# Optimization experiments

Measured on AMD Instinct MI355X. Metric: run time of the kernel, lower is better.

Reference implementation:

```python
import jax, jax.numpy as jnp
import numpy as np

B, N, E = 2, 50000, 800000
IN_CH, SP_CH, OUT_CH, EDGE_CH = 64, 16, 32, 1


def _xavier(k, shape):
    scale = (2.0 / (shape[0] + shape[1])) ** 0.5
    return jax.random.normal(k, shape, dtype=jnp.float32) * scale


def setup_inputs() -> dict:
    key = jax.random.key(0)
    ks = jax.random.split(key, 20)
    return {
        "X": jax.random.normal(ks[0], (B, N, IN_CH), dtype=jnp.float32),
        "edge_index0": jax.random.randint(ks[1], (2, E), 0, N),
        "edge_index1": jax.random.randint(ks[2], (2, E), 0, N),
        "edge_weight0": jax.random.uniform(ks[3], (E, EDGE_CH), dtype=jnp.float32),
        "edge_weight1": jax.random.uniform(ks[4], (E, EDGE_CH), dtype=jnp.float32),
        "res_n_id0": jnp.arange(N),
        "res_n_id1": jnp.arange(N),
        # conv1 params (in=IN_CH, out=SP_CH)
        "value1": _xavier(ks[5], (IN_CH, SP_CH)),
        "key1": _xavier(ks[6], (SP_CH, SP_CH)),
        "query1": _xavier(ks[7], (SP_CH, SP_CH)),
        "we1": _xavier(ks[8], (EDGE_CH, SP_CH)),
        "att_w1": _xavier(ks[9], (3 * SP_CH, 1)),
        "att_b1": jnp.zeros((1,), jnp.float32),
        "cat_w1": _xavier(ks[10], (2 * SP_CH, SP_CH)),
        "cat_b1": jnp.zeros((SP_CH,), jnp.float32),
        # conv2 params (in=SP_CH, out=OUT_CH)
        "value2": _xavier(ks[11], (SP_CH, OUT_CH)),
        "key2": _xavier(ks[12], (OUT_CH, OUT_CH)),
        "query2": _xavier(ks[13], (OUT_CH, OUT_CH)),
        "we2": _xavier(ks[14], (EDGE_CH, OUT_CH)),
        "att_w2": _xavier(ks[15], (3 * OUT_CH, 1)),
        "att_b2": jnp.zeros((1,), jnp.float32),
        "cat_w2": _xavier(ks[16], (2 * OUT_CH, OUT_CH)),
        "cat_b2": jnp.zeros((OUT_CH,), jnp.float32),
    }


def _egnn_conv(Xs, Xd, ei, ef, value, key_w, query_w, we, att_w, att_b, cat_w, cat_b):
    # Xs: [B,Ns,Cin] source nodes, Xd: [B,Nd,Cin] dest nodes, ei: [2,E], ef: [E,edge_ch]
    xs = Xs @ value                       # [B,Ns,C]
    xd = Xd @ value                       # [B,Nd,C]
    e = ef @ we                           # [E,C]
    xj = xs[:, ei[0]]                     # [B,E,C] source gather
    xi = xd[:, ei[1]]                     # [B,E,C] dest gather
    q = xj @ query_w                      # note: original code names are swapped; kept faithful
    k = xi @ key_w
    att_in = jnp.concatenate([k, q, jnp.broadcast_to(e, q.shape)], axis=-1)  # [B,E,3C]
    att = jax.nn.sigmoid(att_in @ att_w + att_b)      # [B,E,1]
    msg = att * xj * jax.nn.sigmoid(e)                # [B,E,C]
    aggr = jnp.zeros(xd.shape, xd.dtype).at[:, ei[1]].add(msg)  # scatter-add over dest
    upd = jnp.concatenate([xd, aggr], axis=-1) @ cat_w + cat_b  # [B,Nd,C]
    return xd + jax.nn.relu(upd)


def reference(X, edge_index0, edge_index1, edge_weight0, edge_weight1,
              res_n_id0, res_n_id1,
              value1, key1, query1, we1, att_w1, att_b1, cat_w1, cat_b1,
              value2, key2, query2, we2, att_w2, att_b2, cat_w2, cat_b2):
    X1 = _egnn_conv(X, X[:, res_n_id0], edge_index0, edge_weight0,
                    value1, key1, query1, we1, att_w1, att_b1, cat_w1, cat_b1)
    X1 = jax.nn.leaky_relu(X1)  # negative_slope 0.01, matches torch default
    X2 = _egnn_conv(X1, X1[:, res_n_id1], edge_index1, edge_weight1,
                    value2, key2, query2, we2, att_w2, att_b2, cat_w2, cat_b2)
    return X2
```

## Files before the change

kernel.cpp:

```cpp
#include <hip/hip_runtime.h>
#include <hip/hip_fp16.h>

#define BB   2
#define NN   50000
#define EE   800000
#define INCH 64
#define C1   16
#define C2   32
#define NB   (BB*NN)

#define W1S   6
#define W2S   5
#define NBK1  ((NN + 63) >> 6)
#define NBK2  ((NN + 31) >> 5)
#define NBKT  (NBK1 + NBK2)
#define EB    4096
#define TPB   1024
#define NEBLK ((2*EE + EB - 1) / EB)

#define OFF_XS1   0
#define OFF_XS2   (OFF_XS1 + NB*C1/2)
#define OFF_DOTK1 (OFF_XS2 + NB*C2/2)
#define OFF_DOTQ1 (OFF_DOTK1 + NB)
#define OFF_DOTK2 (OFF_DOTQ1 + NB)
#define OFF_DOTQ2 (OFF_DOTK2 + NB)
#define OFF_AG1   (OFF_DOTQ2 + NB)
#define OFF_AG2   (OFF_AG1 + NN*32)
#define OFF_BTOT  (OFF_AG2 + NN*64)
#define OFF_BBASE (OFF_BTOT + NBKT)
#define OFF_START (OFF_BBASE + NBKT)
#define OFF_DEG   (OFF_START + 2*NN)
#define OFF_SC    (OFF_DEG + 2*NN)
#define OFF_RECS2 (OFF_SC + 2)
#define OFF_REGION (OFF_RECS2 + 2*EE*2)
#define OFF_RECS   OFF_REGION
#define OFF_BCNT   (OFF_REGION + 2*EE*2)
#define OFF_PREC   OFF_REGION

__device__ __forceinline__ float sigmoidf(float x) {
    return __builtin_amdgcn_rcpf(1.0f + __expf(-x));
}

__global__ void k_sc(const float* __restrict__ we1, const float* __restrict__ aw1,
                     const float* __restrict__ we2, const float* __restrict__ aw2,
                     float* __restrict__ sc) {
    if (threadIdx.x == 0) {
        float e = 0.f;
        for (int j = 0; j < C1; ++j) e += we1[j] * aw1[2*C1+j];
        sc[0] = e;
    }
    if (threadIdx.x == 1) {
        float e = 0.f;
        for (int j = 0; j < C2; ++j) e += we2[j] * aw2[2*C2+j];
        sc[1] = e;
    }
}

__global__ __launch_bounds__(TPB) void k_cnt(
        const int* __restrict__ ei0, const int* __restrict__ ei1,
        unsigned* __restrict__ blockCnt) {
    __shared__ unsigned h[NBKT];
    int tid = threadIdx.x;
    for (int i = tid; i < NBKT; i += TPB) h[i] = 0u;
    __syncthreads();
    int base = blockIdx.x * EB;
#pragma unroll
    for (int j = 0; j < EB/TPB; ++j) {
        int t = base + j*TPB + tid;
        if (t < 2*EE) {
            int bkt;
            if (t < EE) { int dst = ei0[EE + t];      bkt = dst >> W1S; }
            else        { int dst = ei1[EE + t - EE]; bkt = NBK1 + (dst >> W2S); }
            atomicAdd(&h[bkt], 1u);
        }
    }
    __syncthreads();
    unsigned* o = blockCnt + (size_t)blockIdx.x * NBKT;
    for (int i = tid; i < NBKT; i += TPB) o[i] = h[i];
}

__global__ __launch_bounds__(512) void k_scanBkt(
        unsigned* __restrict__ blockCnt, unsigned* __restrict__ bktTot) {
    __shared__ unsigned s[512];
    int tid = threadIdx.x;
    int bkt = blockIdx.x;
    unsigned v = (tid < NEBLK) ? blockCnt[(size_t)tid * NBKT + bkt] : 0u;
    s[tid] = v;
    __syncthreads();
    for (int o = 1; o < 512; o <<= 1) {
        unsigned t = (tid >= o) ? s[tid - o] : 0u;
        __syncthreads();
        s[tid] += t;
        __syncthreads();
    }
    if (tid < NEBLK) blockCnt[(size_t)tid * NBKT + bkt] = s[tid] - v;
    if (tid == 511) bktTot[bkt] = s[511];
}

__global__ __launch_bounds__(1024) void k_scanTot(
        const unsigned* __restrict__ bktTot, unsigned* __restrict__ bucketBase) {
    __shared__ unsigned s[1024];
    int tid = threadIdx.x;
    int base = tid * 3;
    unsigned a0 = (base + 0 < NBKT) ? bktTot[base + 0] : 0u;
    unsigned a1 = (base + 1 < NBKT) ? bktTot[base + 1] : 0u;
    unsigned a2 = (base + 2 < NBKT) ? bktTot[base + 2] : 0u;
    unsigned l = a0 + a1 + a2;
    s[tid] = l;
    __syncthreads();
    for (int o = 1; o < 1024; o <<= 1) {
        unsigned t = (tid >= o) ? s[tid - o] : 0u;
        __syncthreads();
        s[tid] += t;
        __syncthreads();
    }
    unsigned ex = s[tid] - l;
    if (base + 0 < NBKT) bucketBase[base + 0] = ex;
    if (base + 1 < NBKT) bucketBase[base + 1] = ex + a0;
    if (base + 2 < NBKT) bucketBase[base + 2] = ex + a0 + a1;
}

__global__ __launch_bounds__(TPB) void k_permute(
        const int* __restrict__ ei0, const int* __restrict__ ei1,
        const float* __restrict__ ew0, const float* __restrict__ ew1,
        const unsigned* __restrict__ blockOff, const unsigned* __restrict__ bucketBase,
        uint2* __restrict__ recs) {
    __shared__ unsigned off[NBKT];
    __shared__ unsigned cur[NBKT];
    int tid = threadIdx.x;
    const unsigned* bo = blockOff + (size_t)blockIdx.x * NBKT;
    for (int i = tid; i < NBKT; i += TPB) { off[i] = bo[i] + bucketBase[i]; cur[i] = 0u; }
    __syncthreads();
    int base = blockIdx.x * EB;
#pragma unroll
    for (int j = 0; j < EB/TPB; ++j) {
        int t = base + j*TPB + tid;
        if (t >= 2*EE) break;
        int bkt, dl, src; float ef;
        if (t < EE) {
            int dst = ei0[EE + t];
            bkt = dst >> W1S; dl = dst & 63;
            src = ei0[t]; ef = ew0[t];
        } else {
            int e = t - EE;
            int dst = ei1[EE + e];
            bkt = NBK1 + (dst >> W2S); dl = dst & 31;
            src = ei1[e]; ef = ew1[e];
        }
        unsigned pos = off[bkt] + atomicAdd(&cur[bkt], 1u);
        recs[pos] = make_uint2((unsigned)src | ((unsigned)dl << 16), __float_as_uint(ef));
    }
}

__global__ __launch_bounds__(256) void k_sortb(
        const uint2* __restrict__ recs, const unsigned* __restrict__ bktTot,
        const unsigned* __restrict__ bucketBase,
        uint2* __restrict__ recs2, unsigned* __restrict__ startA,
        unsigned* __restrict__ degA) {
    __shared__ unsigned h[64], sOff[64], cur[64];
    int tid = threadIdx.x;
    int bkt = blockIdx.x;
    int lay1 = (bkt < NBK1) ? 1 : 0;
    int ndl  = lay1 ? 64 : 32;
    int nodeBase = lay1 ? (bkt << W1S) : ((bkt - NBK1) << W2S);
    int layOff   = lay1 ? 0 : NN;
    if (tid < 64) h[tid] = 0u;
    __syncthreads();
    unsigned cnt = bktTot[bkt], base = bucketBase[bkt];
    for (unsigned i = tid; i < cnt; i += 256)
        atomicAdd(&h[recs[base + i].x >> 16], 1u);
    __syncthreads();
    if (tid == 0) {
        unsigned run = 0;
        for (int d = 0; d < ndl; ++d) { sOff[d] = run; run += h[d]; }
    }
    __syncthreads();
    if (tid < ndl) {
        cur[tid] = sOff[tid];
        int node = nodeBase + tid;
        if (node < NN) {
            startA[layOff + node] = base + sOff[tid];
            degA[layOff + node]   = h[tid];
        }
    }
    __syncthreads();
    for (unsigned i = tid; i < cnt; i += 256) {
        uint2 r = recs[base + i];
        unsigned dl  = r.x >> 16;
        unsigned src = r.x & 0xffffu;
        unsigned pos = atomicAdd(&cur[dl], 1u);
        unsigned dst = (unsigned)nodeBase + dl;
        recs2[base + pos] = make_uint2(src | (dst << 16), r.y);
    }
}

__global__ __launch_bounds__(256) void k_value1(
        const float* __restrict__ X, const float* __restrict__ value1,
        const float* __restrict__ key1, const float* __restrict__ query1,
        const float* __restrict__ aw1,
        __half* __restrict__ xs1h, float* __restrict__ dotk1, float* __restrict__ dotq1) {
    __shared__ float W[INCH*C1];
    __shared__ float KV[C1], QV[C1];
    int tid = threadIdx.x;
    for (int i = tid; i < INCH*C1; i += 256) W[i] = value1[i];
    if (tid < C1) {
        float kv = 0.f, qv = 0.f;
#pragma unroll
        for (int j = 0; j < C1; ++j) {
            kv += key1[tid*C1+j]   * aw1[j];
            qv += query1[tid*C1+j] * aw1[C1+j];
        }
        KV[tid] = kv; QV[tid] = qv;
    }
    __syncthreads();
    int bn = blockIdx.x * 256 + tid;
    if (bn >= NB) return;
    int b = (bn >= NN) ? 1 : 0;
    int node = bn - b*NN;
    const float4* Xr = (const float4*)(X + (size_t)bn * INCH);
    float acc[C1];
#pragma unroll
    for (int j = 0; j < C1; ++j) acc[j] = 0.f;
#pragma unroll
    for (int v = 0; v < 16; ++v) {
        float4 p = Xr[v];
        float x4[4] = {p.x, p.y, p.z, p.w};
#pragma unroll
        for (int h = 0; h < 4; ++h) {
            int i = v*4 + h;
            float xv = x4[h];
#pragma unroll
            for (int j = 0; j < C1; ++j) acc[j] += xv * W[i*C1+j];
        }
    }
    float dk = 0.f, dq = 0.f;
#pragma unroll
    for (int j = 0; j < C1; ++j) { dk += acc[j]*KV[j]; dq += acc[j]*QV[j]; }
    __half* o = xs1h + ((size_t)node * C1) * 2 + b;
#pragma unroll
    for (int j = 0; j < C1; ++j) o[2*j] = __float2half_rn(acc[j]);
    dotk1[node*2 + b] = dk; dotq1[node*2 + b] = dq;
}

__global__ __launch_bounds__(256) void k_prep(
        const uint2* __restrict__ recs2seg, const float* __restrict__ dotk,
        const float* __restrict__ dotq, const float* __restrict__ ab,
        const float* __restrict__ sc, int scIdx, uint2* __restrict__ prec) {
    int e = blockIdx.x * 256 + threadIdx.x;
    uint2 r = recs2seg[e];
    int src = r.x & 0xffff, dst = r.x >> 16;
    float ef = __uint_as_float(r.y);
    float eb = ef * sc[scIdx] + ab[0];
    float2 dk = *(const float2*)(dotk + dst*2);
    float2 dq = *(const float2*)(dotq + src*2);
    float p0 = sigmoidf(dk.x + dq.x + eb);
    float p1 = sigmoidf(dk.y + dq.y + eb);
    unsigned pu = __builtin_bit_cast(unsigned, __floats2half2_rn(p0, p1));
    unsigned eu = (unsigned)__half_as_ushort(__float2half_rn(ef));
    prec[e] = make_uint2((unsigned)src | (pu << 16),
                         (pu >> 16) | (eu << 16));
}

__global__ __launch_bounds__(256) void k_aggr1f(
        const uint2* __restrict__ prec, const float* __restrict__ we,
        const uint2* __restrict__ xsh,
        const unsigned* __restrict__ startA, const unsigned* __restrict__ degA,
        float* __restrict__ aggrf) {
    int t = blockIdx.x * 256 + threadIdx.x;
    int node = t >> 4, sub = t & 15, cp = sub & 7, h = sub >> 3;
    unsigned s = startA[node];
    unsigned n = degA[node];
    float w0 = we[2*cp], w1 = we[2*cp+1];
    float a0 = 0.f, a1 = 0.f, a2 = 0.f, a3 = 0.f;
    unsigned i = (unsigned)h;
    uint2 r_n = make_uint2(0u, 0u); uint2 xr_n = make_uint2(0u, 0u);
    if (i < n) {
        r_n  = prec[s + i];
        xr_n = xsh[(size_t)(r_n.x & 0xffff)*8 + cp];
    }
    for (; i < n; i += 2) {
        uint2 r = r_n; uint2 xr = xr_n;
        if (i + 2 < n) {
            r_n  = prec[s + i + 2];
            xr_n = xsh[(size_t)(r_n.x & 0xffff)*8 + cp];
        }
        float p0 = __half2float(__ushort_as_half((unsigned short)(r.x >> 16)));
        float p1 = __half2float(__ushort_as_half((unsigned short)(r.y & 0xffff)));
        float ef = __half2float(__ushort_as_half((unsigned short)(r.y >> 16)));
        float se0 = sigmoidf(ef * w0);
        float se1 = sigmoidf(ef * w1);
        float2 f0 = __half22float2(__builtin_bit_cast(__half2, xr.x));
        float2 f1 = __half22float2(__builtin_bit_cast(__half2, xr.y));
        a0 += p0 * se0 * f0.x;
        a1 += p1 * se0 * f0.y;
        a2 += p0 * se1 * f1.x;
        a3 += p1 * se1 * f1.y;
    }
    a0 += __shfl_xor(a0, 8); a1 += __shfl_xor(a1, 8);
    a2 += __shfl_xor(a2, 8); a3 += __shfl_xor(a3, 8);
    if (h == 0)
        ((float4*)aggrf)[(size_t)node*8 + cp] = make_float4(a0, a1, a2, a3);
}

__global__ __launch_bounds__(256) void k_update1(
        const float* __restrict__ cat_w, const float* __restrict__ cat_b,
        const float* __restrict__ value2,
        const float* __restrict__ key2, const float* __restrict__ query2,
        const float* __restrict__ aw2,
        const __half* __restrict__ xs1h, const float* __restrict__ aggr1f,
        __half* __restrict__ xs2h, float* __restrict__ dotk2, float* __restrict__ dotq2) {
    __shared__ float CW[2*C1*C1];
    __shared__ float CB[C1];
    __shared__ float V2[C1*C2];
    __shared__ float KV[C2], QV[C2];
    int tid = threadIdx.x;
    for (int i = tid; i < 2*C1*C1; i += 256) CW[i] = cat_w[i];
    for (int i = tid; i < C1*C2;   i += 256) V2[i] = value2[i];
    if (tid < C1) CB[tid] = cat_b[tid];
    if (tid < C2) {
        float kv = 0.f;
#pragma unroll
        for (int j = 0; j < C2; ++j) kv += key2[tid*C2+j] * aw2[j];
        KV[tid] = kv;
    } else if (tid < 2*C2) {
        int c = tid - C2;
        float qv = 0.f;
#pragma unroll
        for (int j = 0; j < C2; ++j) qv += query2[c*C2+j] * aw2[C2+j];
        QV[c] = qv;
    }
    __syncthreads();
    int bn = blockIdx.x * 256 + tid;
    if (bn >= NB) return;
    int b = (bn >= NN) ? 1 : 0;
    int node = bn - b*NN;
    const __half* xr = xs1h + ((size_t)node*C1)*2 + b;
    const float* agp = aggr1f + (size_t)node*32;
    float xd[C1], ag[C1];
#pragma unroll
    for (int i = 0; i < C1; ++i) xd[i] = __half2float(xr[2*i]);
#pragma unroll
    for (int i = 0; i < C1; ++i) ag[i] = agp[(i>>1)*4 + (i&1)*2 + b];
    float x1[C1];
#pragma unroll
    for (int j = 0; j < C1; ++j) {
        float u = CB[j];
#pragma unroll
        for (int i = 0; i < C1; ++i) {
            u += xd[i] * CW[i*C1 + j];
            u += ag[i] * CW[(C1+i)*C1 + j];
        }
        float o = xd[j] + fmaxf(u, 0.f);
        x1[j] = (o > 0.f) ? o : 0.01f * o;
    }
    float o2[C2];
#pragma unroll
    for (int k = 0; k < C2; ++k) o2[k] = 0.f;
#pragma unroll
    for (int j = 0; j < C1; ++j) {
        float xv = x1[j];
#pragma unroll
        for (int k = 0; k < C2; ++k) o2[k] += xv * V2[j*C2 + k];
    }
    float dk = 0.f, dq = 0.f;
#pragma unroll
    for (int k = 0; k < C2; ++k) { dk += o2[k]*KV[k]; dq += o2[k]*QV[k]; }
    __half* o = xs2h + ((size_t)node*C2)*2 + b;
#pragma unroll
    for (int k = 0; k < C2; ++k) o[2*k] = __float2half_rn(o2[k]);
    dotk2[node*2 + b] = dk; dotq2[node*2 + b] = dq;
}

__global__ __launch_bounds__(256) void k_aggr2f(
        const uint2* __restrict__ prec, const float* __restrict__ we,
        const uint2* __restrict__ xsh,
        const unsigned* __restrict__ startA, const unsigned* __restrict__ degA,
        float* __restrict__ aggrf) {
    int t = blockIdx.x * 256 + threadIdx.x;
    int node = t >> 5, sub = t & 31, cp = sub & 15, h = sub >> 4;
    unsigned s = startA[NN + node] - EE;
    unsigned n = degA[NN + node];
    float w0 = we[2*cp], w1 = we[2*cp+1];
    float a0 = 0.f, a1 = 0.f, a2 = 0.f, a3 = 0.f;
    unsigned i = (unsigned)h;
    uint2 r_n = make_uint2(0u, 0u); uint2 xr_n = make_uint2(0u, 0u);
    if (i < n) {
        r_n  = prec[s + i];
        xr_n = xsh[(size_t)(r_n.x & 0xffff)*16 + cp];
    }
    for (; i < n; i += 2) {
        uint2 r = r_n; uint2 xr = xr_n;
        if (i + 2 < n) {
            r_n  = prec[s + i + 2];
            xr_n = xsh[(size_t)(r_n.x & 0xffff)*16 + cp];
        }
        float p0 = __half2float(__ushort_as_half((unsigned short)(r.x >> 16)));
        float p1 = __half2float(__ushort_as_half((unsigned short)(r.y & 0xffff)));
        float ef = __half2float(__ushort_as_half((unsigned short)(r.y >> 16)));
        float se0 = sigmoidf(ef * w0);
        float se1 = sigmoidf(ef * w1);
        float2 f0 = __half22float2(__builtin_bit_cast(__half2, xr.x));
        float2 f1 = __half22float2(__builtin_bit_cast(__half2, xr.y));
        a0 += p0 * se0 * f0.x;
        a1 += p1 * se0 * f0.y;
        a2 += p0 * se1 * f1.x;
        a3 += p1 * se1 * f1.y;
    }
    a0 += __shfl_xor(a0, 16); a1 += __shfl_xor(a1, 16);
    a2 += __shfl_xor(a2, 16); a3 += __shfl_xor(a3, 16);
    if (h == 0)
        ((float4*)aggrf)[(size_t)node*16 + cp] = make_float4(a0, a1, a2, a3);
}

__global__ __launch_bounds__(256) void k_update2(
        const float* __restrict__ cat_w, const float* __restrict__ cat_b,
        const __half* __restrict__ xs2h, const float* __restrict__ aggr2f,
        float* __restrict__ out) {
    __shared__ float CW[2*C2*C2];
    __shared__ float CB[C2];
    int tid = threadIdx.x;
    for (int i = tid; i < 2*C2*C2; i += 256) CW[i] = cat_w[i];
    if (tid < C2) CB[tid] = cat_b[tid];
    __syncthreads();
    int bn = blockIdx.x * 256 + tid;
    if (bn >= NB) return;
    int b = (bn >= NN) ? 1 : 0;
    int node = bn - b*NN;
    const __half* xr = xs2h + ((size_t)node*C2)*2 + b;
    const float* agp = aggr2f + (size_t)node*64;
    float xd[C2], ag[C2];
#pragma unroll
    for (int i = 0; i < C2; ++i) xd[i] = __half2float(xr[2*i]);
#pragma unroll
    for (int i = 0; i < C2; ++i) ag[i] = agp[(i>>1)*4 + (i&1)*2 + b];
    float o[C2];
#pragma unroll
    for (int k = 0; k < C2; ++k) {
        float u = CB[k];
#pragma unroll
        for (int i = 0; i < C2; ++i) {
            u += xd[i] * CW[i*C2 + k];
            u += ag[i] * CW[(C2+i)*C2 + k];
        }
        o[k] = xd[k] + fmaxf(u, 0.f);
    }
    float4* dst = (float4*)(out + (size_t)bn * C2);
#pragma unroll
    for (int v = 0; v < 8; ++v)
        dst[v] = make_float4(o[4*v], o[4*v+1], o[4*v+2], o[4*v+3]);
}

extern "C" void kernel_launch(void* const* d_in, const int* in_sizes, int n_in,
                              void* d_out, int out_size, void* d_ws, size_t ws_size,
                              hipStream_t stream) {
    const float* X      = (const float*)d_in[0];
    const int*   ei0    = (const int*)d_in[1];
    const int*   ei1    = (const int*)d_in[2];
    const float* ew0    = (const float*)d_in[3];
    const float* ew1    = (const float*)d_in[4];
    const float* value1 = (const float*)d_in[7];
    const float* key1   = (const float*)d_in[8];
    const float* query1 = (const float*)d_in[9];
    const float* we1    = (const float*)d_in[10];
    const float* aw1    = (const float*)d_in[11];
    const float* ab1    = (const float*)d_in[12];
    const float* cw1    = (const float*)d_in[13];
    const float* cb1    = (const float*)d_in[14];
    const float* value2 = (const float*)d_in[15];
    const float* key2   = (const float*)d_in[16];
    const float* query2 = (const float*)d_in[17];
    const float* we2    = (const float*)d_in[18];
    const float* aw2    = (const float*)d_in[19];
    const float* ab2    = (const float*)d_in[20];
    const float* cw2    = (const float*)d_in[21];
    const float* cb2    = (const float*)d_in[22];
    float* ws  = (float*)d_ws;
    float* out = (float*)d_out;

    __half* xs1h = (__half*)(ws + OFF_XS1);
    __half* xs2h = (__half*)(ws + OFF_XS2);
    float* aggr1f = ws + OFF_AG1;
    float* aggr2f = ws + OFF_AG2;
    unsigned* blockCnt   = (unsigned*)(ws + OFF_BCNT);
    unsigned* bktTot     = (unsigned*)(ws + OFF_BTOT);
    unsigned* bucketBase = (unsigned*)(ws + OFF_BBASE);
    unsigned* startA     = (unsigned*)(ws + OFF_START);
    unsigned* degA       = (unsigned*)(ws + OFF_DEG);
    uint2*    recs2      = (uint2*)(ws + OFF_RECS2);
    uint2*    recs       = (uint2*)(ws + OFF_RECS);
    uint2*    prec       = (uint2*)(ws + OFF_PREC);

    k_sc<<<1, 64, 0, stream>>>(we1, aw1, we2, aw2, ws + OFF_SC);

    k_value1<<<(NB+255)/256, 256, 0, stream>>>(X, value1, key1, query1, aw1,
                                               xs1h, ws + OFF_DOTK1, ws + OFF_DOTQ1);

    k_cnt<<<NEBLK, TPB, 0, stream>>>(ei0, ei1, blockCnt);
    k_scanBkt<<<NBKT, 512, 0, stream>>>(blockCnt, bktTot);
    k_scanTot<<<1, 1024, 0, stream>>>(bktTot, bucketBase);
    k_permute<<<NEBLK, TPB, 0, stream>>>(ei0, ei1, ew0, ew1,
                                         blockCnt, bucketBase, recs);
    k_sortb<<<NBKT, 256, 0, stream>>>(recs, bktTot, bucketBase,
                                      recs2, startA, degA);

    k_prep<<<EE/256, 256, 0, stream>>>(recs2, ws + OFF_DOTK1, ws + OFF_DOTQ1,
                                       ab1, ws + OFF_SC, 0, prec);
    k_aggr1f<<<(NN*16)/256, 256, 0, stream>>>(prec, we1, (const uint2*)xs1h,
                                              startA, degA, aggr1f);
    k_update1<<<(NB+255)/256, 256, 0, stream>>>(cw1, cb1, value2, key2, query2, aw2,
                                                xs1h, aggr1f,
                                                xs2h, ws + OFF_DOTK2, ws + OFF_DOTQ2);

    k_prep<<<EE/256, 256, 0, stream>>>(recs2 + EE, ws + OFF_DOTK2, ws + OFF_DOTQ2,
                                       ab2, ws + OFF_SC, 1, prec);
    k_aggr2f<<<(NN*32)/256, 256, 0, stream>>>(prec, we2, (const uint2*)xs2h,
                                              startA, degA, aggr2f);
    k_update2<<<(NB+255)/256, 256, 0, stream>>>(cw2, cb2, xs2h, aggr2f, out);
}
```

Before: 325.3 us.

## Fuse value1 projection into edge counting and layer-1 prep into bucket sort

The node projection, the scalar setup and the per-bucket edge histogram now run in one launch. Within each block, 256 threads compute the node projection while the other 768 build the histogram. The layer-1 attention precompute (sigmoid gates packed as half2 plus the edge feature) is folded into the second sort pass, which writes final packed records straight into recs2. This drops two kernel launches and a full read/write pass over the layer-1 edge records. In exchange, the sort kernel does extra gathers of dotk and dotq, and the fused first kernel has divergent roles inside each block.

```diff
diff --git a/kernel.cpp b/kernel.cpp
--- a/kernel.cpp
+++ b/kernel.cpp
@@ -41,37 +41,84 @@
     return __builtin_amdgcn_rcpf(1.0f + __expf(-x));
 }
 
-__global__ void k_sc(const float* __restrict__ we1, const float* __restrict__ aw1,
-                     const float* __restrict__ we2, const float* __restrict__ aw2,
-                     float* __restrict__ sc) {
-    if (threadIdx.x == 0) {
-        float e = 0.f;
-        for (int j = 0; j < C1; ++j) e += we1[j] * aw1[2*C1+j];
-        sc[0] = e;
-    }
-    if (threadIdx.x == 1) {
-        float e = 0.f;
-        for (int j = 0; j < C2; ++j) e += we2[j] * aw2[2*C2+j];
-        sc[1] = e;
-    }
-}
-
-__global__ __launch_bounds__(TPB) void k_cnt(
+__global__ __launch_bounds__(TPB) void k_value1cnt(
+        const float* __restrict__ X, const float* __restrict__ value1,
+        const float* __restrict__ key1, const float* __restrict__ query1,
+        const float* __restrict__ aw1,
         const int* __restrict__ ei0, const int* __restrict__ ei1,
-        unsigned* __restrict__ blockCnt) {
+        const float* __restrict__ we1, const float* __restrict__ we2,
+        const float* __restrict__ aw2,
+        __half* __restrict__ xs1h, float* __restrict__ dotk1,
+        float* __restrict__ dotq1, unsigned* __restrict__ blockCnt,
+        float* __restrict__ sc) {
+    __shared__ float W[INCH*C1];
+    __shared__ float KV[C1], QV[C1];
     __shared__ unsigned h[NBKT];
     int tid = threadIdx.x;
-    for (int i = tid; i < NBKT; i += TPB) h[i] = 0u;
-    __syncthreads();
-    int base = blockIdx.x * EB;
-#pragma unroll
-    for (int j = 0; j < EB/TPB; ++j) {
-        int t = base + j*TPB + tid;
-        if (t < 2*EE) {
-            int bkt;
-            if (t < EE) { int dst = ei0[EE + t];      bkt = dst >> W1S; }
-            else        { int dst = ei1[EE + t - EE]; bkt = NBK1 + (dst >> W2S); }
-            atomicAdd(&h[bkt], 1u);
+    if (tid < 256) {
+        for (int i = tid; i < INCH*C1; i += 256) W[i] = value1[i];
+        if (tid < C1) {
+            float kv = 0.f, qv = 0.f;
+#pragma unroll
+            for (int j = 0; j < C1; ++j) {
+                kv += key1[tid*C1+j]   * aw1[j];
+                qv += query1[tid*C1+j] * aw1[C1+j];
+            }
+            KV[tid] = kv; QV[tid] = qv;
+        }
+    } else {
+        for (int i = tid - 256; i < NBKT; i += 768) h[i] = 0u;
+        if (blockIdx.x == 0 && tid == 256) {
+            float e = 0.f;
+            for (int j = 0; j < C1; ++j) e += we1[j] * aw1[2*C1+j];
+            sc[0] = e;
+        }
+        if (blockIdx.x == 0 && tid == 257) {
+            float e = 0.f;
+            for (int j = 0; j < C2; ++j) e += we2[j] * aw2[2*C2+j];
+            sc[1] = e;
+        }
+    }
+    __syncthreads();
+    if (tid < 256) {
+        int bn = blockIdx.x * 256 + tid;
+        if (bn < NB) {
+            int b = (bn >= NN) ? 1 : 0;
+            int node = bn - b*NN;
+            const float4* Xr = (const float4*)(X + (size_t)bn * INCH);
+            float acc[C1];
+#pragma unroll
+            for (int j = 0; j < C1; ++j) acc[j] = 0.f;
+#pragma unroll
+            for (int v = 0; v < 16; ++v) {
+                float4 p = Xr[v];
+                float x4[4] = {p.x, p.y, p.z, p.w};
+#pragma unroll
+                for (int hh = 0; hh < 4; ++hh) {
+                    int i = v*4 + hh;
+                    float xv = x4[hh];
+#pragma unroll
+                    for (int j = 0; j < C1; ++j) acc[j] += xv * W[i*C1+j];
+                }
+            }
+            float dk = 0.f, dq = 0.f;
+#pragma unroll
+            for (int j = 0; j < C1; ++j) { dk += acc[j]*KV[j]; dq += acc[j]*QV[j]; }
+            __half* o = xs1h + ((size_t)node * C1) * 2 + b;
+#pragma unroll
+            for (int j = 0; j < C1; ++j) o[2*j] = __float2half_rn(acc[j]);
+            dotk1[node*2 + b] = dk; dotq1[node*2 + b] = dq;
+        }
+    } else {
+        int base = blockIdx.x * EB;
+        for (int j = tid - 256; j < EB; j += 768) {
+            int t = base + j;
+            if (t < 2*EE) {
+                int bkt;
+                if (t < EE) { int dst = ei0[EE + t];      bkt = dst >> W1S; }
+                else        { int dst = ei1[EE + t - EE]; bkt = NBK1 + (dst >> W2S); }
+                atomicAdd(&h[bkt], 1u);
+            }
         }
     }
     __syncthreads();
@@ -152,9 +199,11 @@
     }
 }
 
-__global__ __launch_bounds__(256) void k_sortb(
+__global__ __launch_bounds__(256) void k_sortbp(
         const uint2* __restrict__ recs, const unsigned* __restrict__ bktTot,
         const unsigned* __restrict__ bucketBase,
+        const float* __restrict__ dotk1, const float* __restrict__ dotq1,
+        const float* __restrict__ ab1, const float* __restrict__ sc,
         uint2* __restrict__ recs2, unsigned* __restrict__ startA,
         unsigned* __restrict__ degA) {
     __shared__ unsigned h[64], sOff[64], cur[64];
@@ -184,62 +233,28 @@
         }
     }
     __syncthreads();
+    float ec = sc[0], ab0 = ab1[0];
     for (unsigned i = tid; i < cnt; i += 256) {
         uint2 r = recs[base + i];
         unsigned dl  = r.x >> 16;
         unsigned src = r.x & 0xffffu;
         unsigned pos = atomicAdd(&cur[dl], 1u);
         unsigned dst = (unsigned)nodeBase + dl;
-        recs2[base + pos] = make_uint2(src | (dst << 16), r.y);
-    }
-}
-
-__global__ __launch_bounds__(256) void k_value1(
-        const float* __restrict__ X, const float* __restrict__ value1,
-        const float* __restrict__ key1, const float* __restrict__ query1,
-        const float* __restrict__ aw1,
-        __half* __restrict__ xs1h, float* __restrict__ dotk1, float* __restrict__ dotq1) {
-    __shared__ float W[INCH*C1];
-    __shared__ float KV[C1], QV[C1];
-    int tid = threadIdx.x;
-    for (int i = tid; i < INCH*C1; i += 256) W[i] = value1[i];
-    if (tid < C1) {
-        float kv = 0.f, qv = 0.f;
-#pragma unroll
-        for (int j = 0; j < C1; ++j) {
-            kv += key1[tid*C1+j]   * aw1[j];
-            qv += query1[tid*C1+j] * aw1[C1+j];
-        }
-        KV[tid] = kv; QV[tid] = qv;
-    }
-    __syncthreads();
-    int bn = blockIdx.x * 256 + tid;
-    if (bn >= NB) return;
-    int b = (bn >= NN) ? 1 : 0;
-    int node = bn - b*NN;
-    const float4* Xr = (const float4*)(X + (size_t)bn * INCH);
-    float acc[C1];
-#pragma unroll
-    for (int j = 0; j < C1; ++j) acc[j] = 0.f;
-#pragma unroll
-    for (int v = 0; v < 16; ++v) {
-        float4 p = Xr[v];
-        float x4[4] = {p.x, p.y, p.z, p.w};
-#pragma unroll
-        for (int h = 0; h < 4; ++h) {
-            int i = v*4 + h;
-            float xv = x4[h];
-#pragma unroll
-            for (int j = 0; j < C1; ++j) acc[j] += xv * W[i*C1+j];
-        }
-    }
-    float dk = 0.f, dq = 0.f;
-#pragma unroll
-    for (int j = 0; j < C1; ++j) { dk += acc[j]*KV[j]; dq += acc[j]*QV[j]; }
-    __half* o = xs1h + ((size_t)node * C1) * 2 + b;
-#pragma unroll
-    for (int j = 0; j < C1; ++j) o[2*j] = __float2half_rn(acc[j]);
-    dotk1[node*2 + b] = dk; dotq1[node*2 + b] = dq;
+        if (lay1) {
+            float ef = __uint_as_float(r.y);
+            float eb = ef * ec + ab0;
+            float2 dk = *(const float2*)(dotk1 + dst*2);
+            float2 dq = *(const float2*)(dotq1 + src*2);
+            float p0 = sigmoidf(dk.x + dq.x + eb);
+            float p1 = sigmoidf(dk.y + dq.y + eb);
+            unsigned pu = __builtin_bit_cast(unsigned, __floats2half2_rn(p0, p1));
+            unsigned eu = (unsigned)__half_as_ushort(__float2half_rn(ef));
+            recs2[base + pos] = make_uint2(src | (pu << 16),
+                                           (pu >> 16) | (eu << 16));
+        } else {
+            recs2[base + pos] = make_uint2(src | (dst << 16), r.y);
+        }
+    }
 }
 
 __global__ __launch_bounds__(256) void k_prep(
@@ -488,32 +503,31 @@
     unsigned* degA       = (unsigned*)(ws + OFF_DEG);
     uint2*    recs2      = (uint2*)(ws + OFF_RECS2);
     uint2*    recs       = (uint2*)(ws + OFF_RECS);
-    uint2*    prec       = (uint2*)(ws + OFF_PREC);
-
-    k_sc<<<1, 64, 0, stream>>>(we1, aw1, we2, aw2, ws + OFF_SC);
-
-    k_value1<<<(NB+255)/256, 256, 0, stream>>>(X, value1, key1, query1, aw1,
-                                               xs1h, ws + OFF_DOTK1, ws + OFF_DOTQ1);
-
-    k_cnt<<<NEBLK, TPB, 0, stream>>>(ei0, ei1, blockCnt);
+    uint2*    prec2      = (uint2*)(ws + OFF_PREC);
+
+    k_value1cnt<<<NEBLK, TPB, 0, stream>>>(X, value1, key1, query1, aw1,
+                                           ei0, ei1, we1, we2, aw2,
+                                           xs1h, ws + OFF_DOTK1, ws + OFF_DOTQ1,
+                                           blockCnt, ws + OFF_SC);
+
     k_scanBkt<<<NBKT, 512, 0, stream>>>(blockCnt, bktTot);
     k_scanTot<<<1, 1024, 0, stream>>>(bktTot, bucketBase);
     k_permute<<<NEBLK, TPB, 0, stream>>>(ei0, ei1, ew0, ew1,
                                          blockCnt, bucketBase, recs);
-    k_sortb<<<NBKT, 256, 0, stream>>>(recs, bktTot, bucketBase,
-                                      recs2, startA, degA);
-
-    k_prep<<<EE/256, 256, 0, stream>>>(recs2, ws + OFF_DOTK1, ws + OFF_DOTQ1,
-                                       ab1, ws + OFF_SC, 0, prec);
-    k_aggr1f<<<(NN*16)/256, 256, 0, stream>>>(prec, we1, (const uint2*)xs1h,
+    k_sortbp<<<NBKT, 256, 0, stream>>>(recs, bktTot, bucketBase,
+                                       ws + OFF_DOTK1, ws + OFF_DOTQ1,
+                                       ab1, ws + OFF_SC,
+                                       recs2, startA, degA);
+
+    k_aggr1f<<<(NN*16)/256, 256, 0, stream>>>(recs2, we1, (const uint2*)xs1h,
                                               startA, degA, aggr1f);
     k_update1<<<(NB+255)/256, 256, 0, stream>>>(cw1, cb1, value2, key2, query2, aw2,
                                                 xs1h, aggr1f,
                                                 xs2h, ws + OFF_DOTK2, ws + OFF_DOTQ2);
 
     k_prep<<<EE/256, 256, 0, stream>>>(recs2 + EE, ws + OFF_DOTK2, ws + OFF_DOTQ2,
-                                       ab2, ws + OFF_SC, 1, prec);
-    k_aggr2f<<<(NN*32)/256, 256, 0, stream>>>(prec, we2, (const uint2*)xs2h,
+                                       ab2, ws + OFF_SC, 1, prec2);
+    k_aggr2f<<<(NN*32)/256, 256, 0, stream>>>(prec2, we2, (const uint2*)xs2h,
                                               startA, degA, aggr2f);
     k_update2<<<(NB+255)/256, 256, 0, stream>>>(cw2, cb2, xs2h, aggr2f, out);
 }
```

New measurement: 314.5 us. 1.03x faster.
